# Optimization experiments

Measured on AMD Instinct MI355X. Metric: run time of the kernel, lower is better.

Reference implementation:

```python
import jax, jax.numpy as jnp
import numpy as np

N_NODES = 50000
N_EDGES = 800000
D_IN = 64
D_HID = 128  # out_channels * expansion(2)
EPS_MSG = 1e-7
EPS_SOFTMAX = 1e-16
EPS_BN = 1e-5
N_LAYERS = 4


def mish(x):
    return x * jnp.tanh(jax.nn.softplus(x))


def setup_inputs() -> dict:
    key = jax.random.key(0)
    ks = jax.random.split(key, 8)
    x = jax.random.normal(ks[0], (N_NODES, D_IN), dtype=jnp.float32)
    edge_index = jax.random.randint(ks[1], (2, N_EDGES), 0, N_NODES, dtype=jnp.int64)
    # Per-layer GENConv MLP params: Linear(64->128), BN(128), ReLU, Linear(128->64)
    s1 = 1.0 / np.sqrt(D_IN)
    s2 = 1.0 / np.sqrt(D_HID)
    W1 = jax.random.uniform(ks[2], (N_LAYERS, D_IN, D_HID), jnp.float32, -s1, s1)
    b1 = jax.random.uniform(ks[3], (N_LAYERS, D_HID), jnp.float32, -s1, s1)
    gamma = jnp.ones((N_LAYERS, D_HID), jnp.float32)
    beta = jnp.zeros((N_LAYERS, D_HID), jnp.float32)
    W2 = jax.random.uniform(ks[4], (N_LAYERS, D_HID, D_IN), jnp.float32, -s2, s2)
    b2 = jax.random.uniform(ks[5], (N_LAYERS, D_IN), jnp.float32, -s2, s2)
    return {"x": x, "edge_index": edge_index, "W1": W1, "b1": b1,
            "gamma": gamma, "beta": beta, "W2": W2, "b2": b2}


def gen_conv(x, src, dst, W1, b1, gamma, beta, W2, b2):
    n = x.shape[0]
    # message: relu(x_j) + eps  -> [E, D]
    msg = jax.nn.relu(x[src]) + EPS_MSG
    # softmax aggregation (t=1) per destination node, per feature channel
    m = jax.ops.segment_max(msg, dst, num_segments=n)
    e = jnp.exp(msg - m[dst])
    denom = jax.ops.segment_sum(e, dst, num_segments=n)[dst] + EPS_SOFTMAX
    alpha = e / denom
    agg = jax.ops.segment_sum(msg * alpha, dst, num_segments=n)
    # residual with destination features, then 2-layer MLP w/ BatchNorm (train mode)
    h = agg + x
    h = h @ W1 + b1
    mu = jnp.mean(h, axis=0)
    var = jnp.var(h, axis=0)  # biased, as torch BN uses for normalization
    h = (h - mu) * jax.lax.rsqrt(var + EPS_BN) * gamma + beta
    h = jax.nn.relu(h)
    return h @ W2 + b2


def reference(x, edge_index, W1, b1, gamma, beta, W2, b2):
    src, dst = edge_index[0], edge_index[1]
    h = x
    for i in range(N_LAYERS):
        h = gen_conv(h, src, dst, W1[i], b1[i], gamma[i], beta[i], W2[i], b2[i])
        if i < N_LAYERS - 1:
            h = mish(h)
    return h
```

## Files before the change

### kernel.cpp

```cpp
#include <hip/hip_runtime.h>
#include <math.h>

#define N_NODES 50000
#define N_EDGES 800000
#define D_IN 64
#define D_HID 128
#define SCAN_B 256
#define N_SB ((N_NODES + SCAN_B - 1) / SCAN_B)
#define NPB 256
#define NB ((N_NODES + NPB - 1) / NPB)
#define P1_BLOCKS 256
#define EPB (N_EDGES / P1_BLOCKS)

typedef unsigned short u16;
typedef unsigned int u32;
typedef __attribute__((ext_vector_type(8))) short short8;
typedef __attribute__((ext_vector_type(4))) float f32x4;

union U4S8 { uint4 u; short8 s; };

__device__ __forceinline__ float bf2f(u16 u) {
    u32 x = ((u32)u) << 16;
    float f; __builtin_memcpy(&f, &x, 4); return f;
}
__device__ __forceinline__ u16 f2bf(float f) {
    u32 x; __builtin_memcpy(&x, &f, 4);
    x += 0x7fffu + ((x >> 16) & 1u);
    return (u16)(x >> 16);
}
__device__ __forceinline__ u32 pk2(float a, float b) {
    return (u32)f2bf(a) | ((u32)f2bf(b) << 16);
}
__device__ __forceinline__ u32 relu2(u32 w) {
    u32 b = (w >> 15) & 0x00010001u;
    u32 m01 = b ^ 0x00010001u;
    u32 M = (m01 << 16) - m01;
    return w & M;
}


__global__ void count_kernel(const int* __restrict__ dst, int* __restrict__ deg, int E) {
    int i = blockIdx.x * blockDim.x + threadIdx.x;
    if (i < E) atomicAdd(&deg[dst[i]], 1);
}

__global__ __launch_bounds__(SCAN_B) void scan_reduce_kernel(const int* __restrict__ deg,
                                                             int* __restrict__ bsum) {
    __shared__ int s[SCAN_B];
    int i = blockIdx.x * SCAN_B + threadIdx.x;
    int v = (i < N_NODES) ? deg[i] : 0;
    s[threadIdx.x] = v;
    __syncthreads();
    #pragma unroll
    for (int o = SCAN_B / 2; o > 0; o >>= 1) {
        if (threadIdx.x < o) s[threadIdx.x] += s[threadIdx.x + o];
        __syncthreads();
    }
    if (threadIdx.x == 0) bsum[blockIdx.x] = s[0];
}

__global__ __launch_bounds__(SCAN_B) void scan_sums_kernel(const int* __restrict__ bsum,
                                                           int* __restrict__ boff) {
    __shared__ int s[SCAN_B];
    int t = threadIdx.x;
    int v = (t < N_SB) ? bsum[t] : 0;
    s[t] = v;
    __syncthreads();
    #pragma unroll
    for (int o = 1; o < SCAN_B; o <<= 1) {
        int u = (t >= o) ? s[t - o] : 0;
        __syncthreads();
        s[t] += u;
        __syncthreads();
    }
    if (t < N_SB) boff[t] = s[t] - v;
}

__global__ __launch_bounds__(SCAN_B) void scan_write_kernel(const int* __restrict__ deg,
                                                            const int* __restrict__ boff,
                                                            int* __restrict__ off) {
    __shared__ int s[SCAN_B];
    int t = threadIdx.x;
    int i = blockIdx.x * SCAN_B + t;
    int v = (i < N_NODES) ? deg[i] : 0;
    s[t] = v;
    __syncthreads();
    #pragma unroll
    for (int o = 1; o < SCAN_B; o <<= 1) {
        int u = (t >= o) ? s[t - o] : 0;
        __syncthreads();
        s[t] += u;
        __syncthreads();
    }
    int incl = s[t] + boff[blockIdx.x];
    if (i < N_NODES) off[i] = incl - v;
    if (i == N_NODES - 1) off[N_NODES] = incl;
}

__global__ void bin_init_kernel(const int* __restrict__ off, int* __restrict__ gcur) {
    int b = threadIdx.x;
    if (b < NB) gcur[b] = off[min(b * NPB, N_NODES)];
}

__global__ __launch_bounds__(256) void bin_pass1_kernel(const int* __restrict__ src,
                                                        const int* __restrict__ dst,
                                                        int* __restrict__ gcur,
                                                        int2* __restrict__ ebuf) {
    __shared__ int hist[NB];
    __shared__ int base[NB];
    const int tid = threadIdx.x;
    const int e0 = blockIdx.x * EPB, e1 = e0 + EPB;
    for (int b = tid; b < NB; b += 256) hist[b] = 0;
    __syncthreads();
    for (int i = e0 + tid; i < e1; i += 256)
        atomicAdd(&hist[dst[i] >> 8], 1);
    __syncthreads();
    for (int b = tid; b < NB; b += 256) {
        base[b] = atomicAdd(&gcur[b], hist[b]);
        hist[b] = 0;
    }
    __syncthreads();
    for (int i = e0 + tid; i < e1; i += 256) {
        int d = dst[i];
        int b = d >> 8;
        int slot = base[b] + atomicAdd(&hist[b], 1);
        ebuf[slot] = make_int2(src[i], d);
    }
}

__global__ __launch_bounds__(256) void bin_pass2_kernel(const int* __restrict__ off,
                                                        const int2* __restrict__ ebuf,
                                                        int* __restrict__ esrc) {
    __shared__ int soff[NPB];
    __shared__ int cur[NPB];
    const int b = blockIdx.x;
    const int tid = threadIdx.x;
    const int n0 = b * NPB;
    soff[tid] = off[min(n0 + tid, N_NODES)];
    cur[tid] = 0;
    __syncthreads();
    const int e0 = soff[0];
    const int e1 = off[min(n0 + NPB, N_NODES)];
    for (int i = e0 + tid; i < e1; i += 256) {
        int2 p = ebuf[i];
        int dl = p.y - n0;
        int slot = soff[dl] + atomicAdd(&cur[dl], 1);
        esrc[slot] = p.x;
    }
}

__global__ __launch_bounds__(256) void xcvt_kernel(const float* __restrict__ x,
                                                   u16* __restrict__ xb,
                                                   u16* __restrict__ rb) {
    int i = blockIdx.x * 256 + threadIdx.x;
    if (i < N_NODES * D_IN / 4) {
        float4 v = ((const float4*)x)[i];
        u32 lo = pk2(v.x, v.y), hi = pk2(v.z, v.w);
        ((uint2*)xb)[i] = make_uint2(lo, hi);
        ((uint2*)rb)[i] = make_uint2(relu2(lo), relu2(hi));
    }
}

__global__ __launch_bounds__(256) void wprep_kernel(const float* __restrict__ W1,
                                                    const float* __restrict__ W2,
                                                    u16* __restrict__ w1f,
                                                    u16* __restrict__ w2f) {
    const int b = blockIdx.x;
    const int L = b >> 1;
    if ((b & 1) == 0) {
        const float* W = W1 + (size_t)L * 64 * 128;
        u16* outp = w1f + (size_t)L * 8192;
        for (int idx = threadIdx.x; idx < 1024; idx += 256) {
            int ln = idx & 63, th = idx >> 6;
            int half = th & 1, t = th >> 1;
            int k0 = half * 32 + (ln >> 4) * 8;
            int n = t * 16 + (ln & 15);
            uint4 o;
            o.x = pk2(W[(k0 + 0) * 128 + n], W[(k0 + 1) * 128 + n]);
            o.y = pk2(W[(k0 + 2) * 128 + n], W[(k0 + 3) * 128 + n]);
            o.z = pk2(W[(k0 + 4) * 128 + n], W[(k0 + 5) * 128 + n]);
            o.w = pk2(W[(k0 + 6) * 128 + n], W[(k0 + 7) * 128 + n]);
            *(uint4*)&outp[(size_t)idx * 8] = o;
        }
    } else {
        const float* W = W2 + (size_t)L * 128 * 64;
        u16* outp = w2f + (size_t)L * 8192;
        for (int idx = threadIdx.x; idx < 1024; idx += 256) {
            int ln = idx & 63, th = idx >> 6;
            int ks = th & 3, t = th >> 2;
            int k0 = ks * 32 + (ln >> 4) * 8;
            int n = t * 16 + (ln & 15);
            uint4 o;
            o.x = pk2(W[(k0 + 0) * 64 + n], W[(k0 + 1) * 64 + n]);
            o.y = pk2(W[(k0 + 2) * 64 + n], W[(k0 + 3) * 64 + n]);
            o.z = pk2(W[(k0 + 4) * 64 + n], W[(k0 + 5) * 64 + n]);
            o.w = pk2(W[(k0 + 6) * 64 + n], W[(k0 + 7) * 64 + n]);
            *(uint4*)&outp[(size_t)idx * 8] = o;
        }
    }
}

__global__ __launch_bounds__(256) void agg_kernel(const u16* __restrict__ xb,
                                                  const u16* __restrict__ rb,
                                                  const int* __restrict__ off,
                                                  const int* __restrict__ esrc,
                                                  u16* __restrict__ h) {
    const int node = blockIdx.x * 4 + (threadIdx.x >> 6);
    const int ln = threadIdx.x & 63;
    const int e = ln >> 3;
    const int cb = (ln & 7) * 8;
    if (node >= N_NODES) return;
    const int jb = off[node], je = off[node + 1];
    U4S8 xr;
    xr.u = *(const uint4*)&xb[(size_t)node * D_IN + cb];
    float s[8], t[8];
    #pragma unroll
    for (int k = 0; k < 8; k++) { s[k] = 0.f; t[k] = 0.f; }
    int j = jb;
    for (; j + 16 <= je; j += 16) {
        int i0 = esrc[j + e];
        int i1 = esrc[j + 8 + e];
        U4S8 r0, r1;
        r0.u = *(const uint4*)&rb[(size_t)i0 * D_IN + cb];
        r1.u = *(const uint4*)&rb[(size_t)i1 * D_IN + cb];
        #pragma unroll
        for (int k = 0; k < 8; k++) {
            float m = bf2f((u16)r0.s[k]);
            float p = __expf(m);
            s[k] += p; t[k] = fmaf(m, p, t[k]);
        }
        #pragma unroll
        for (int k = 0; k < 8; k++) {
            float m = bf2f((u16)r1.s[k]);
            float p = __expf(m);
            s[k] += p; t[k] = fmaf(m, p, t[k]);
        }
    }
    int rem = je - j;
    if (rem > 0) {
        bool act = e < rem;
        int idx = esrc[j + (act ? e : rem - 1)];
        U4S8 r;
        r.u = *(const uint4*)&rb[(size_t)idx * D_IN + cb];
        if (act) {
            #pragma unroll
            for (int k = 0; k < 8; k++) {
                float m = bf2f((u16)r.s[k]);
                float p = __expf(m);
                s[k] += p; t[k] = fmaf(m, p, t[k]);
            }
        }
        if (rem > 8) {
            bool act2 = (e + 8) < rem;
            int idx2 = esrc[j + 8 + (act2 ? e : rem - 9)];
            U4S8 r2;
            r2.u = *(const uint4*)&rb[(size_t)idx2 * D_IN + cb];
            if (act2) {
                #pragma unroll
                for (int k = 0; k < 8; k++) {
                    float m = bf2f((u16)r2.s[k]);
                    float p = __expf(m);
                    s[k] += p; t[k] = fmaf(m, p, t[k]);
                }
            }
        }
    }
    #pragma unroll
    for (int k = 0; k < 8; k++) {
        s[k] += __shfl_xor(s[k], 8);
        s[k] += __shfl_xor(s[k], 16);
        s[k] += __shfl_xor(s[k], 32);
        t[k] += __shfl_xor(t[k], 8);
        t[k] += __shfl_xor(t[k], 16);
        t[k] += __shfl_xor(t[k], 32);
    }
    if (e == 0) {
        u32 w[4];
        #pragma unroll
        for (int k2 = 0; k2 < 4; k2++) {
            float v0 = t[2 * k2]     / (s[2 * k2]     + 1e-16f) + 1e-7f + bf2f((u16)xr.s[2 * k2]);
            float v1 = t[2 * k2 + 1] / (s[2 * k2 + 1] + 1e-16f) + 1e-7f + bf2f((u16)xr.s[2 * k2 + 1]);
            w[k2] = pk2(v0, v1);
        }
        *(uint4*)&h[(size_t)node * D_IN + cb] = make_uint4(w[0], w[1], w[2], w[3]);
    }
}

#define SC1 136
__global__ __launch_bounds__(256) void gemm1_kernel(const u16* __restrict__ A,
                                                    const u16* __restrict__ Wf,
                                                    const float* __restrict__ bias,
                                                    u16* __restrict__ Bout,
                                                    float* __restrict__ S,
                                                    float* __restrict__ Q) {
    __shared__ u16 sC[64 * SC1];
    __shared__ float sRed[2][4][128];
    const int tid = threadIdx.x;
    const int wave = tid >> 6, ln = tid & 63;
    const int lm = ln & 15, quad = ln >> 4;
    const int row0g = blockIdx.x * 64;
    const int row0 = row0g + wave * 16;
    const int rA = min(row0 + lm, N_NODES - 1);

    U4S8 a0, a1;
    a0.u = *(const uint4*)&A[(size_t)rA * 64 + quad * 8];
    a1.u = *(const uint4*)&A[(size_t)rA * 64 + 32 + quad * 8];

    f32x4 acc[8];
    #pragma unroll
    for (int t = 0; t < 8; t++) {
        float b = bias[t * 16 + lm];
        acc[t] = (f32x4){b, b, b, b};
    }
    #pragma unroll
    for (int t = 0; t < 8; t++) {
        U4S8 b0, b1;
        b0.u = *(const uint4*)&Wf[(size_t)((t * 2 + 0) * 64 + ln) * 8];
        b1.u = *(const uint4*)&Wf[(size_t)((t * 2 + 1) * 64 + ln) * 8];
        acc[t] = __builtin_amdgcn_mfma_f32_16x16x32_bf16(a0.s, b0.s, acc[t], 0, 0, 0);
        acc[t] = __builtin_amdgcn_mfma_f32_16x16x32_bf16(a1.s, b1.s, acc[t], 0, 0, 0);
    }
    const int rbase = row0 + quad * 4;
    #pragma unroll
    for (int t = 0; t < 8; t++) {
        float ss = 0.f, qq = 0.f;
        #pragma unroll
        for (int rg = 0; rg < 4; rg++) {
            if (rbase + rg < N_NODES) {
                float v = acc[t][rg];
                ss += v; qq = fmaf(v, v, qq);
            }
        }
        ss += __shfl_xor(ss, 16); ss += __shfl_xor(ss, 32);
        qq += __shfl_xor(qq, 16); qq += __shfl_xor(qq, 32);
        if (quad == 0) {
            sRed[0][wave][t * 16 + lm] = ss;
            sRed[1][wave][t * 16 + lm] = qq;
        }
    }
    const int lr0 = wave * 16 + quad * 4;
    #pragma unroll
    for (int t = 0; t < 8; t++) {
        #pragma unroll
        for (int rg = 0; rg < 4; rg++)
            sC[(lr0 + rg) * SC1 + t * 16 + lm] = f2bf(acc[t][rg]);
    }
    __syncthreads();
    const int c8 = (tid & 15) * 8;
    #pragma unroll
    for (int i = 0; i < 4; i++) {
        int lr = (tid >> 4) + i * 16;
        int r = row0g + lr;
        if (r < N_NODES)
            *(uint4*)&Bout[(size_t)r * 128 + c8] = *(const uint4*)&sC[lr * SC1 + c8];
    }
    if (tid < 128) {
        float v = sRed[0][0][tid] + sRed[0][1][tid] + sRed[0][2][tid] + sRed[0][3][tid];
        atomicAdd(&S[tid], v);
    } else {
        int c = tid - 128;
        float v = sRed[1][0][c] + sRed[1][1][c] + sRed[1][2][c] + sRed[1][3][c];
        atomicAdd(&Q[c], v);
    }
}

__device__ __forceinline__ float mish_f(float v) {
    if (v > 30.f) return v;
    float u = __expf(v);
    float t = (u + 1.f) * (u + 1.f);
    return v * (t - 1.f) / (t + 1.f);
}

#define SC2B 72
#define SC2F 68
__global__ __launch_bounds__(256) void gemm2_kernel(const u16* __restrict__ H,
                                                    const float* __restrict__ S,
                                                    const float* __restrict__ Q,
                                                    const float* __restrict__ gamma,
                                                    const float* __restrict__ beta,
                                                    const u16* __restrict__ Wf,
                                                    const float* __restrict__ bias,
                                                    float* __restrict__ outf,
                                                    u16* __restrict__ xb,
                                                    u16* __restrict__ rb,
                                                    int dobf16) {
    __shared__ float sss[256];
    __shared__ __align__(16) char sCraw[64 * SC2F * 4];
    u16* sCb = (u16*)sCraw;
    float* sCf = (float*)sCraw;
    const int tid = threadIdx.x;
    if (tid < 128) {
        float mean = S[tid] * (1.f / N_NODES);
        float var = fmaxf(Q[tid] * (1.f / N_NODES) - mean * mean, 0.f);
        float sc = gamma[tid] * rsqrtf(var + 1e-5f);
        sss[tid] = sc;
        sss[128 + tid] = beta[tid] - mean * sc;
    }
    __syncthreads();
    const int wave = tid >> 6, ln = tid & 63;
    const int lm = ln & 15, quad = ln >> 4;
    const int row0g = blockIdx.x * 64;
    const int row0 = row0g + wave * 16;
    const int rA = min(row0 + lm, N_NODES - 1);

    f32x4 acc[4];
    #pragma unroll
    for (int t = 0; t < 4; t++) {
        float b = bias[t * 16 + lm];
        acc[t] = (f32x4){b, b, b, b};
    }
    #pragma unroll
    for (int ks = 0; ks < 4; ks++) {
        const int k0 = ks * 32 + quad * 8;
        U4S8 h8;
        h8.u = *(const uint4*)&H[(size_t)rA * 128 + k0];
        U4S8 a;
        #pragma unroll
        for (int j2 = 0; j2 < 4; j2++) {
            int k = k0 + 2 * j2;
            float v0 = fmaxf(fmaf(bf2f((u16)h8.s[2 * j2]),     sss[k],     sss[128 + k]),     0.f);
            float v1 = fmaxf(fmaf(bf2f((u16)h8.s[2 * j2 + 1]), sss[k + 1], sss[128 + k + 1]), 0.f);
            ((u32*)&a.u)[j2] = pk2(v0, v1);
        }
        #pragma unroll
        for (int t = 0; t < 4; t++) {
            U4S8 b;
            b.u = *(const uint4*)&Wf[(size_t)((t * 4 + ks) * 64 + ln) * 8];
            acc[t] = __builtin_amdgcn_mfma_f32_16x16x32_bf16(a.s, b.s, acc[t], 0, 0, 0);
        }
    }
    const int lr0 = wave * 16 + quad * 4;
    if (dobf16) {
        #pragma unroll
        for (int t = 0; t < 4; t++) {
            #pragma unroll
            for (int rg = 0; rg < 4; rg++)
                sCb[(lr0 + rg) * SC2B + t * 16 + lm] = f2bf(mish_f(acc[t][rg]));
        }
        __syncthreads();
        const int c8 = (tid & 7) * 8;
        #pragma unroll
        for (int i = 0; i < 2; i++) {
            int lr = (tid >> 3) + i * 32;
            int r = row0g + lr;
            if (r < N_NODES) {
                uint4 val = *(const uint4*)&sCb[lr * SC2B + c8];
                *(uint4*)&xb[(size_t)r * 64 + c8] = val;
                uint4 rv;
                rv.x = relu2(val.x); rv.y = relu2(val.y);
                rv.z = relu2(val.z); rv.w = relu2(val.w);
                *(uint4*)&rb[(size_t)r * 64 + c8] = rv;
            }
        }
    } else {
        #pragma unroll
        for (int t = 0; t < 4; t++) {
            #pragma unroll
            for (int rg = 0; rg < 4; rg++)
                sCf[(lr0 + rg) * SC2F + t * 16 + lm] = acc[t][rg];
        }
        __syncthreads();
        const int c8 = (tid & 7) * 8;
        #pragma unroll
        for (int i = 0; i < 2; i++) {
            int lr = (tid >> 3) + i * 32;
            int r = row0g + lr;
            if (r < N_NODES) {
                *(float4*)&outf[(size_t)r * 64 + c8]     = *(const float4*)&sCf[lr * SC2F + c8];
                *(float4*)&outf[(size_t)r * 64 + c8 + 4] = *(const float4*)&sCf[lr * SC2F + c8 + 4];
            }
        }
    }
}


extern "C" void kernel_launch(void* const* d_in, const int* in_sizes, int n_in,
                              void* d_out, int out_size, void* d_ws, size_t ws_size,
                              hipStream_t stream) {
    const float* x     = (const float*)d_in[0];
    const int*   ei    = (const int*)d_in[1];
    const float* W1    = (const float*)d_in[2];
    const float* b1    = (const float*)d_in[3];
    const float* gamma = (const float*)d_in[4];
    const float* beta  = (const float*)d_in[5];
    const float* W2    = (const float*)d_in[6];
    const float* b2    = (const float*)d_in[7];
    float* out = (float*)d_out;

    const int* src = ei;
    const int* dst = ei + N_EDGES;

    char* base = (char*)d_ws;
    size_t o = 0;
    auto take = [&](size_t bytes) -> char* {
        char* p = base + o;
        o = (o + bytes + 255) & ~(size_t)255;
        return p;
    };
    int* deg     = (int*)take((size_t)N_NODES * 4);
    int* off     = (int*)take((size_t)(N_NODES + 1) * 4);
    int* esrc    = (int*)take((size_t)N_EDGES * 4);
    int2* ebuf   = (int2*)take((size_t)N_EDGES * 8);
    int* bsum    = (int*)take((size_t)N_SB * 4);
    int* boff    = (int*)take((size_t)N_SB * 4);
    int* gcur    = (int*)take((size_t)NB * 4);
    float* bn    = (float*)take(1024 * 4);
    u16* w1f     = (u16*)take((size_t)4 * 8192 * 2);
    u16* w2f     = (u16*)take((size_t)4 * 8192 * 2);
    u16* xbuf    = (u16*)take((size_t)N_NODES * D_IN * 2);
    u16* rbuf    = (u16*)take((size_t)N_NODES * D_IN * 2);
    u16* hbuf    = (u16*)take((size_t)N_NODES * D_IN * 2);
    u16* h1buf   = (u16*)take((size_t)N_NODES * D_HID * 2);

    hipMemsetAsync(deg, 0, (size_t)N_NODES * 4, stream);
    hipMemsetAsync(bn, 0, 1024 * 4, stream);
    count_kernel<<<(N_EDGES + 255) / 256, 256, 0, stream>>>(dst, deg, N_EDGES);
    scan_reduce_kernel<<<N_SB, SCAN_B, 0, stream>>>(deg, bsum);
    scan_sums_kernel<<<1, SCAN_B, 0, stream>>>(bsum, boff);
    scan_write_kernel<<<N_SB, SCAN_B, 0, stream>>>(deg, boff, off);
    bin_init_kernel<<<1, 256, 0, stream>>>(off, gcur);
    bin_pass1_kernel<<<P1_BLOCKS, 256, 0, stream>>>(src, dst, gcur, ebuf);
    bin_pass2_kernel<<<NB, 256, 0, stream>>>(off, ebuf, esrc);
    xcvt_kernel<<<(N_NODES * D_IN / 4 + 255) / 256, 256, 0, stream>>>(x, xbuf, rbuf);
    wprep_kernel<<<8, 256, 0, stream>>>(W1, W2, w1f, w2f);

    const int NBLK = (N_NODES + 63) / 64;
    const int ABLK = (N_NODES + 3) / 4;
    for (int L = 0; L < 4; L++) {
        float* Sb = bn + L * 256;
        float* Qb = Sb + 128;
        agg_kernel<<<ABLK, 256, 0, stream>>>(xbuf, rbuf, off, esrc, hbuf);
        gemm1_kernel<<<NBLK, 256, 0, stream>>>(
            hbuf, w1f + (size_t)L * 8192, b1 + (size_t)L * D_HID, h1buf,
            Sb, Qb);
        gemm2_kernel<<<NBLK, 256, 0, stream>>>(
            h1buf, Sb, Qb, gamma + (size_t)L * D_HID, beta + (size_t)L * D_HID,
            w2f + (size_t)L * 8192, b2 + (size_t)L * D_IN,
            out, xbuf, rbuf, (L < 3) ? 1 : 0);
    }
}
```

Measured before the change: 433.9 us.

## Remap aggregation so each lane owns one feature channel across all edges

The aggregation kernel now gives each wave one node and each lane one of its 64 feature channels. Edge indices are read as wave-uniform scalars, and each neighbour row is fetched as a single 128-byte coalesced bf16 row. This removes the 8x8 edge/channel split, the cross-lane shuffle reduction and the single-lane masked store. The tail is handled with a padded esrc buffer and predicated exps, and the node bound check is dropped, which relies on N_NODES being divisible by 4. In exchange, each lane now issues 2-byte scalar loads instead of 16-byte vector loads, so memory instruction count rises.

```diff
diff --git a/kernel.cpp b/kernel.cpp
--- a/kernel.cpp
+++ b/kernel.cpp
@@ -97,9 +97,11 @@
     if (i == N_NODES - 1) off[N_NODES] = incl;
 }
 
-__global__ void bin_init_kernel(const int* __restrict__ off, int* __restrict__ gcur) {
+__global__ void bin_init_kernel(const int* __restrict__ off, int* __restrict__ gcur,
+                                int* __restrict__ esrc) {
     int b = threadIdx.x;
     if (b < NB) gcur[b] = off[min(b * NPB, N_NODES)];
+    if (b < 16) esrc[N_EDGES + b] = 0;
 }
 
 __global__ __launch_bounds__(256) void bin_pass1_kernel(const int* __restrict__ src,
@@ -207,83 +209,42 @@
                                                   u16* __restrict__ h) {
     const int node = blockIdx.x * 4 + (threadIdx.x >> 6);
     const int ln = threadIdx.x & 63;
-    const int e = ln >> 3;
-    const int cb = (ln & 7) * 8;
-    if (node >= N_NODES) return;
-    const int jb = off[node], je = off[node + 1];
-    U4S8 xr;
-    xr.u = *(const uint4*)&xb[(size_t)node * D_IN + cb];
-    float s[8], t[8];
-    #pragma unroll
-    for (int k = 0; k < 8; k++) { s[k] = 0.f; t[k] = 0.f; }
+    const int jb = __builtin_amdgcn_readfirstlane(off[node]);
+    const int je = __builtin_amdgcn_readfirstlane(off[node + 1]);
+    const float xown = bf2f(xb[(size_t)node * 64 + ln]);
+    float s0 = 0.f, s1 = 0.f, t0 = 0.f, t1 = 0.f;
     int j = jb;
-    for (; j + 16 <= je; j += 16) {
-        int i0 = esrc[j + e];
-        int i1 = esrc[j + 8 + e];
-        U4S8 r0, r1;
-        r0.u = *(const uint4*)&rb[(size_t)i0 * D_IN + cb];
-        r1.u = *(const uint4*)&rb[(size_t)i1 * D_IN + cb];
-        #pragma unroll
-        for (int k = 0; k < 8; k++) {
-            float m = bf2f((u16)r0.s[k]);
-            float p = __expf(m);
-            s[k] += p; t[k] = fmaf(m, p, t[k]);
-        }
-        #pragma unroll
-        for (int k = 0; k < 8; k++) {
-            float m = bf2f((u16)r1.s[k]);
-            float p = __expf(m);
-            s[k] += p; t[k] = fmaf(m, p, t[k]);
-        }
-    }
-    int rem = je - j;
+    const int nfull = (je - jb) >> 4;
+    for (int it = 0; it < nfull; ++it, j += 16) {
+        #pragma unroll
+        for (int kk = 0; kk < 16; kk += 2) {
+            int i0 = esrc[j + kk];
+            int i1 = esrc[j + kk + 1];
+            float m0 = bf2f(rb[(size_t)i0 * 64 + ln]);
+            float m1 = bf2f(rb[(size_t)i1 * 64 + ln]);
+            float p0 = __expf(m0);
+            float p1 = __expf(m1);
+            s0 += p0; t0 = fmaf(m0, p0, t0);
+            s1 += p1; t1 = fmaf(m1, p1, t1);
+        }
+    }
+    const int rem = je - j;
     if (rem > 0) {
-        bool act = e < rem;
-        int idx = esrc[j + (act ? e : rem - 1)];
-        U4S8 r;
-        r.u = *(const uint4*)&rb[(size_t)idx * D_IN + cb];
-        if (act) {
-            #pragma unroll
-            for (int k = 0; k < 8; k++) {
-                float m = bf2f((u16)r.s[k]);
-                float p = __expf(m);
-                s[k] += p; t[k] = fmaf(m, p, t[k]);
-            }
-        }
-        if (rem > 8) {
-            bool act2 = (e + 8) < rem;
-            int idx2 = esrc[j + 8 + (act2 ? e : rem - 9)];
-            U4S8 r2;
-            r2.u = *(const uint4*)&rb[(size_t)idx2 * D_IN + cb];
-            if (act2) {
-                #pragma unroll
-                for (int k = 0; k < 8; k++) {
-                    float m = bf2f((u16)r2.s[k]);
-                    float p = __expf(m);
-                    s[k] += p; t[k] = fmaf(m, p, t[k]);
-                }
-            }
-        }
-    }
-    #pragma unroll
-    for (int k = 0; k < 8; k++) {
-        s[k] += __shfl_xor(s[k], 8);
-        s[k] += __shfl_xor(s[k], 16);
-        s[k] += __shfl_xor(s[k], 32);
-        t[k] += __shfl_xor(t[k], 8);
-        t[k] += __shfl_xor(t[k], 16);
-        t[k] += __shfl_xor(t[k], 32);
-    }
-    if (e == 0) {
-        u32 w[4];
-        #pragma unroll
-        for (int k2 = 0; k2 < 4; k2++) {
-            float v0 = t[2 * k2]     / (s[2 * k2]     + 1e-16f) + 1e-7f + bf2f((u16)xr.s[2 * k2]);
-            float v1 = t[2 * k2 + 1] / (s[2 * k2 + 1] + 1e-16f) + 1e-7f + bf2f((u16)xr.s[2 * k2 + 1]);
-            w[k2] = pk2(v0, v1);
-        }
-        *(uint4*)&h[(size_t)node * D_IN + cb] = make_uint4(w[0], w[1], w[2], w[3]);
-    }
+        #pragma unroll
+        for (int kk = 0; kk < 16; kk += 2) {
+            int i0 = esrc[j + kk];
+            int i1 = esrc[j + kk + 1];
+            float m0 = bf2f(rb[(size_t)i0 * 64 + ln]);
+            float m1 = bf2f(rb[(size_t)i1 * 64 + ln]);
+            float p0 = (kk < rem)     ? __expf(m0) : 0.f;
+            float p1 = (kk + 1 < rem) ? __expf(m1) : 0.f;
+            s0 += p0; t0 = fmaf(m0, p0, t0);
+            s1 += p1; t1 = fmaf(m1, p1, t1);
+        }
+    }
+    const float s = s0 + s1, t = t0 + t1;
+    const float v = t / (s + 1e-16f) + 1e-7f + xown;
+    h[(size_t)node * 64 + ln] = f2bf(v);
 }
 
 #define SC1 136
@@ -499,7 +460,7 @@
     };
     int* deg     = (int*)take((size_t)N_NODES * 4);
     int* off     = (int*)take((size_t)(N_NODES + 1) * 4);
-    int* esrc    = (int*)take((size_t)N_EDGES * 4);
+    int* esrc    = (int*)take((size_t)(N_EDGES + 16) * 4);
     int2* ebuf   = (int2*)take((size_t)N_EDGES * 8);
     int* bsum    = (int*)take((size_t)N_SB * 4);
     int* boff    = (int*)take((size_t)N_SB * 4);
@@ -518,7 +479,7 @@
     scan_reduce_kernel<<<N_SB, SCAN_B, 0, stream>>>(deg, bsum);
     scan_sums_kernel<<<1, SCAN_B, 0, stream>>>(bsum, boff);
     scan_write_kernel<<<N_SB, SCAN_B, 0, stream>>>(deg, boff, off);
-    bin_init_kernel<<<1, 256, 0, stream>>>(off, gcur);
+    bin_init_kernel<<<1, 256, 0, stream>>>(off, gcur, esrc);
     bin_pass1_kernel<<<P1_BLOCKS, 256, 0, stream>>>(src, dst, gcur, ebuf);
     bin_pass2_kernel<<<NB, 256, 0, stream>>>(off, ebuf, esrc);
     xcvt_kernel<<<(N_NODES * D_IN / 4 + 255) / 256, 256, 0, stream>>>(x, xbuf, rbuf);
```

New measurement: 400.6 us. 1.08x faster.
